# Optimization experiments

Measured on AMD Instinct MI355X. Metric: run time of the kernel, lower is better.

Reference implementation:

```python
import jax, jax.numpy as jnp
import numpy as np

B, SQ, SKV, D, H = 2, 2048, 2048, 1024, 16
DH = D // H


def setup_inputs() -> dict:
    key = jax.random.key(0)
    ks = jax.random.split(key, 4)
    s = 0.02
    return {
        "query_input": jax.random.normal(ks[0], (B, SQ, D), jnp.float32),
        "kv_input": jax.random.normal(ks[1], (B, SKV, D), jnp.float32),
        "Wq": jax.random.normal(ks[2], (D, D), jnp.float32) * s,
        "bq": jnp.zeros((D,), jnp.float32),
        "Wkv": jax.random.normal(ks[3], (D, 2 * D), jnp.float32) * s,
        "bkv": jnp.zeros((2 * D,), jnp.float32),
        "Wo": jax.random.normal(jax.random.fold_in(key, 7), (D, D), jnp.float32) * s,
        "bo": jnp.zeros((D,), jnp.float32),
    }


def reference(query_input, kv_input, Wq, bq, Wkv, bkv, Wo, bo):
    scale = 1.0 / jnp.sqrt(jnp.float32(DH))
    # Projections
    q = query_input @ Wq + bq                      # [B, SQ, D]
    kv = kv_input @ Wkv + bkv                      # [B, SKV, 2D]
    k, v = jnp.split(kv, 2, axis=-1)               # [B, SKV, D] each
    # Split heads: [B, H, S, DH]
    q = q.reshape(B, SQ, H, DH).transpose(0, 2, 1, 3)
    k = k.reshape(B, SKV, H, DH).transpose(0, 2, 1, 3)
    v = v.reshape(B, SKV, H, DH).transpose(0, 2, 1, 3)
    # Scores S = QK^T / sqrt(d_k)
    scores = jnp.einsum("bhqd,bhkd->bhqk", q, k) * scale
    attn = jax.nn.softmax(scores, axis=-1)
    out = jnp.einsum("bhqk,bhkd->bhqd", attn, v)   # [B, H, SQ, DH]
    out = out.transpose(0, 2, 1, 3).reshape(B, SQ, D)
    return out @ Wo + bo
```

## Files before the change

### kernel.cpp

```cpp
#include <hip/hip_runtime.h>

typedef unsigned short u16;
typedef unsigned int u32;
typedef __bf16 bf16x8 __attribute__((ext_vector_type(8)));
typedef __bf16 bf16x2 __attribute__((ext_vector_type(2)));
typedef float f32x4 __attribute__((ext_vector_type(4)));
typedef float f32x16 __attribute__((ext_vector_type(16)));

#define QSCALE 0.18033688011112f

__device__ __forceinline__ u16 f2bf(float f) {
  u32 u = __builtin_bit_cast(u32, f);
  u += 0x7fffu + ((u >> 16) & 1u);
  return (u16)(u >> 16);
}

__device__ __forceinline__ u32 pkbf(float a, float b) {
  bf16x2 t = {(__bf16)a, (__bf16)b};
  return __builtin_bit_cast(u32, t);
}

__device__ __forceinline__ bf16x8 as_bf16x8(uint4 v) {
  return __builtin_bit_cast(bf16x8, v);
}

__device__ __forceinline__ void async16(const void* g, void* l) {
  __builtin_amdgcn_global_load_lds(
      (__attribute__((address_space(1))) void*)(g),
      (__attribute__((address_space(3))) void*)(l), 16, 0, 0);
}

__global__ void prep_kernel(const float* __restrict__ xq, const float* __restrict__ xkv,
                            const float* __restrict__ Wq, const float* __restrict__ Wkv,
                            const float* __restrict__ Wo,
                            u16* __restrict__ Xq16, u16* __restrict__ Xkv16,
                            u16* __restrict__ WqT, u16* __restrict__ WkvT,
                            u16* __restrict__ WoT) {
  const int bid = blockIdx.x, tid = threadIdx.x;
  if (bid < 8192) {
    int i = bid * 256 + tid;
    const float* s; u16* d; int j;
    if (i < 1048576) { s = xq; d = Xq16; j = i; }
    else             { s = xkv; d = Xkv16; j = i - 1048576; }
    float4 v = ((const float4*)s)[j];
    ushort4 o;
    o.x = f2bf(v.x); o.y = f2bf(v.y); o.z = f2bf(v.z); o.w = f2bf(v.w);
    ((ushort4*)d)[j] = o;
    return;
  }
  const int b2 = bid - 8192;
  const int z = b2 >> 11, rem = b2 & 2047;
  const int by = rem >> 6, bx = rem & 63;
  const float* src; u16* dst; int Nd;
  if (z == 0)      { src = Wq;  dst = WqT;  Nd = 1024; }
  else if (z == 1) { src = Wkv; dst = WkvT; Nd = 2048; }
  else             { src = Wo;  dst = WoT;  Nd = 1024; }
  const int n0 = bx * 32, k0 = by * 32;
  if (n0 >= Nd) return;
  __shared__ float tile[32][33];
  const int tx = tid & 31, ty = tid >> 5;
#pragma unroll
  for (int j = 0; j < 4; ++j)
    tile[ty + 8 * j][tx] = src[(size_t)(k0 + ty + 8 * j) * Nd + n0 + tx];
  __syncthreads();
#pragma unroll
  for (int j = 0; j < 4; ++j)
    dst[(size_t)(n0 + ty + 8 * j) * 1024 + k0 + tx] = f2bf(tile[tx][ty + 8 * j]);
}

template <int MI>
static __device__ __forceinline__ void gemm_core(
    const u16* __restrict__ A, const u16* __restrict__ Bt, int m0,
    uint4* sA, uint4* sB, f32x4 (*acc)[4]) {
  const int tid = threadIdx.x;
  const int wv = tid >> 6, lane = tid & 63;
  const int quad = lane >> 4, l16 = lane & 15;
  const int wm = (wv >> 1) * (MI * 16), wn = (wv & 1) * 64;

  const int ib0 = wv * 128 + lane, ib1 = ib0 + 64;
  const int br0 = ib0 >> 2, bc0 = (ib0 & 3) ^ ((br0 >> 1) & 3);
  const int br1 = ib1 >> 2, bc1 = (ib1 & 3) ^ ((br1 >> 1) & 3);
  const u16* gB0 = Bt + (size_t)br0 * 1024 + bc0 * 8;
  const u16* gB1 = Bt + (size_t)br1 * 1024 + bc1 * 8;

  const int ia0 = wv * (MI * 32) + lane;
  const int ar0 = ia0 >> 2, ac0 = (ia0 & 3) ^ ((ar0 >> 1) & 3);
  const u16* gA0 = A + (size_t)(m0 + ar0) * 1024 + ac0 * 8;
  const int ia1 = ia0 + 64;
  const int ar1 = ia1 >> 2, ac1 = (ia1 & 3) ^ ((ar1 >> 1) & 3);
  const u16* gA1 = A + (size_t)(m0 + ar1) * 1024 + ac1 * 8;
  uint4* sAw = sA + wv * (MI * 32);
  uint4* sBw = sB + wv * 128;

  for (int k0 = 0; k0 < 1024; k0 += 32) {
    __syncthreads();
    async16(gA0 + k0, sAw);
    if (MI == 4) async16(gA1 + k0, sAw + 64);
    async16(gB0 + k0, sBw);
    async16(gB1 + k0, sBw + 64);
    __syncthreads();

    bf16x8 af[MI], bfr[4];
#pragma unroll
    for (int mi = 0; mi < MI; ++mi) {
      int r = wm + mi * 16 + l16;
      af[mi] = as_bf16x8(sA[r * 4 + (quad ^ ((r >> 1) & 3))]);
    }
#pragma unroll
    for (int ni = 0; ni < 4; ++ni) {
      int r = wn + ni * 16 + l16;
      bfr[ni] = as_bf16x8(sB[r * 4 + (quad ^ ((r >> 1) & 3))]);
    }
#pragma unroll
    for (int mi = 0; mi < MI; ++mi)
#pragma unroll
      for (int ni = 0; ni < 4; ++ni)
        acc[mi][ni] = __builtin_amdgcn_mfma_f32_16x16x32_bf16(
            af[mi], bfr[ni], acc[mi][ni], 0, 0, 0);
  }
}

__global__ __launch_bounds__(256, 3) void gemm_qkv(
    const u16* __restrict__ Xq, const u16* __restrict__ Xkv,
    const u16* __restrict__ WqT, const u16* __restrict__ WkvT,
    const float* __restrict__ bq, const float* __restrict__ bkv,
    u16* __restrict__ Qd, u16* __restrict__ Kd, u16* __restrict__ Vd) {
  __shared__ uint4 sA[512], sB[512];
  f32x4 acc[4][4] = {};
  const int n0 = blockIdx.x * 128, m0 = blockIdx.y * 128;
  const u16* A = (n0 < 1024) ? Xq : Xkv;
  const u16* Bt = (n0 < 1024) ? (WqT + (size_t)n0 * 1024)
                              : (WkvT + (size_t)(n0 - 1024) * 1024);
  const float* bias = (n0 < 1024) ? (bq + n0) : (bkv + (n0 - 1024));
  gemm_core<4>(A, Bt, m0, sA, sB, acc);

  const int tid = threadIdx.x, wv = tid >> 6, lane = tid & 63;
  const int quad = lane >> 4, l16 = lane & 15;
  const int wm = (wv >> 1) * 64, wn = (wv & 1) * 64;
  const int bb = m0 >> 11;
  const int gmb = m0 + wm + quad * 4;
  const int ssb = (m0 & 2047) + wm + quad * 4;
#pragma unroll
  for (int ni = 0; ni < 4; ++ni) {
    const int gn = n0 + wn + ni * 16 + l16;
    const float bvn = bias[wn + ni * 16 + l16];
    if (gn < 1024) {
      u16* base = Qd + gn;
#pragma unroll
      for (int mi = 0; mi < 4; ++mi)
#pragma unroll
        for (int r = 0; r < 4; ++r)
          base[(size_t)(gmb + mi * 16 + r) * 1024] = f2bf((acc[mi][ni][r] + bvn) * QSCALE);
    } else if (gn < 2048) {
      u16* base = Kd + (gn - 1024);
#pragma unroll
      for (int mi = 0; mi < 4; ++mi)
#pragma unroll
        for (int r = 0; r < 4; ++r)
          base[(size_t)(gmb + mi * 16 + r) * 1024] = f2bf(acc[mi][ni][r] + bvn);
    } else {
      const int col = gn - 2048, hh = col >> 6, dh = col & 63;
      u16* base = Vd + ((size_t)(bb * 16 + hh) * 64 + dh) * 2048 + ssb;
#pragma unroll
      for (int mi = 0; mi < 4; ++mi) {
        ushort4 o;
        o.x = f2bf(acc[mi][ni][0] + bvn);
        o.y = f2bf(acc[mi][ni][1] + bvn);
        o.z = f2bf(acc[mi][ni][2] + bvn);
        o.w = f2bf(acc[mi][ni][3] + bvn);
        *(ushort4*)(base + mi * 16) = o;
      }
    }
  }
}

__global__ __launch_bounds__(512, 4) void flash_attn(
    const u16* __restrict__ Q, const u16* __restrict__ K,
    const u16* __restrict__ V, u16* __restrict__ O) {
  __shared__ uint4 sbuf[4096];
  __shared__ float sLB[128];
  __shared__ float sLA[128];

  const int tid = threadIdx.x;
  const int wv = tid >> 6, lane = tid & 63;
  const int grp = wv >> 2, wq = wv & 3;
  const int c = lane & 31, hh = lane >> 5;
  const int hb = blockIdx.x & 31;
  const int q0 = (blockIdx.x >> 5) * 128;
  const int h = hb & 15, bz = hb >> 4;

  const u16* Qb = Q + ((size_t)(bz * 2048 + q0 + wq * 32)) * 1024 + h * 64;
  const u16* Kb = K + ((size_t)(bz * 2048 + grp * 64)) * 1024 + h * 64;
  const u16* Vb = V + ((size_t)(bz * 16 + h)) * 64 * 2048 + grp * 64;

  uint4* sKg = sbuf + grp * 1024;
  uint4* sVg = sbuf + 2048 + grp * 1024;

  const int i0 = wq * 128 + lane, i1 = i0 + 64;
  const int r0 = i0 >> 3, r1 = i1 >> 3;
  const int ck0 = (i0 & 7) ^ (r0 & 7), ck1 = (i1 & 7) ^ (r1 & 7);
  const u16* gK0 = Kb + (size_t)r0 * 1024 + ck0 * 8;
  const u16* gK1 = Kb + (size_t)r1 * 1024 + ck1 * 8;
  const u16* gV0 = Vb + (size_t)r0 * 2048 + ck0 * 8;
  const u16* gV1 = Vb + (size_t)r1 * 2048 + ck1 * 8;
  const int wo = wq * 128;

  bf16x8 qf[4];
  {
    const u16* qr = Qb + (size_t)c * 1024 + hh * 8;
#pragma unroll
    for (int s = 0; s < 4; ++s)
      qf[s] = as_bf16x8(*(const uint4*)(qr + 16 * s));
  }

  f32x16 oacc[2] = {};
  float lp = 0.f;

  async16(gK0, sKg + wo);
  async16(gK1, sKg + wo + 64);
  async16(gV0, sVg + wo);
  async16(gV1, sVg + wo + 64);

  for (int t = 0; t < 16; ++t) {
    const int cur = t & 1;
    __syncthreads();
    if (t < 15) {
      const size_t ko = (size_t)(t + 1) * 128 * 1024;
      const int vo = (t + 1) * 128;
      async16(gK0 + ko, sKg + (cur ^ 1) * 512 + wo);
      async16(gK1 + ko, sKg + (cur ^ 1) * 512 + wo + 64);
      async16(gV0 + vo, sVg + (cur ^ 1) * 512 + wo);
      async16(gV1 + vo, sVg + (cur ^ 1) * 512 + wo + 64);
    }
    const uint4* K_ = sKg + cur * 512;
    const uint4* V_ = sVg + cur * 512;

    bf16x8 kf[2][4];
#pragma unroll
    for (int b = 0; b < 2; ++b) {
      const int row = 32 * b + c, sw = row & 7;
#pragma unroll
      for (int s = 0; s < 4; ++s)
        kf[b][s] = as_bf16x8(K_[row * 8 + ((2 * s + hh) ^ sw)]);
    }

    bf16x8 pa[4];
#pragma unroll
    for (int b = 0; b < 2; ++b) {
      f32x16 sAcc = {};
      __builtin_amdgcn_s_setprio(1);
#pragma unroll
      for (int s = 0; s < 4; ++s)
        sAcc = __builtin_amdgcn_mfma_f32_32x32x16_bf16(kf[b][s], qf[s], sAcc, 0, 0, 0);
      __builtin_amdgcn_s_setprio(0);
      float e[16];
#pragma unroll
      for (int r = 0; r < 16; ++r) e[r] = __builtin_amdgcn_exp2f(sAcc[r]);
      float t0 = (e[0] + e[1]) + (e[2] + e[3]);
      float t1 = (e[4] + e[5]) + (e[6] + e[7]);
      float t2 = (e[8] + e[9]) + (e[10] + e[11]);
      float t3 = (e[12] + e[13]) + (e[14] + e[15]);
      lp += (t0 + t1) + (t2 + t3);
      u32 wA0 = pkbf(e[0], e[1]),   wA1 = pkbf(e[2], e[3]);
      u32 wB0 = pkbf(e[4], e[5]),   wB1 = pkbf(e[6], e[7]);
      u32 wC0 = pkbf(e[8], e[9]),   wC1 = pkbf(e[10], e[11]);
      u32 wD0 = pkbf(e[12], e[13]), wD1 = pkbf(e[14], e[15]);
      asm("v_permlane32_swap_b32 %0, %1" : "+v"(wA0), "+v"(wB0));
      asm("v_permlane32_swap_b32 %0, %1" : "+v"(wA1), "+v"(wB1));
      asm("v_permlane32_swap_b32 %0, %1" : "+v"(wC0), "+v"(wD0));
      asm("v_permlane32_swap_b32 %0, %1" : "+v"(wC1), "+v"(wD1));
      uint4 f0 = {wA0, wA1, wB0, wB1};
      uint4 f1 = {wC0, wC1, wD0, wD1};
      pa[2 * b]     = as_bf16x8(f0);
      pa[2 * b + 1] = as_bf16x8(f1);
    }

    bf16x8 vf[2][4];
#pragma unroll
    for (int nb = 0; nb < 2; ++nb) {
      const int row = 32 * nb + c, sw = row & 7;
#pragma unroll
      for (int ks = 0; ks < 4; ++ks)
        vf[nb][ks] = as_bf16x8(V_[row * 8 + ((2 * ks + hh) ^ sw)]);
    }

    __builtin_amdgcn_s_setprio(1);
#pragma unroll
    for (int nb = 0; nb < 2; ++nb)
#pragma unroll
      for (int ks = 0; ks < 4; ++ks)
        oacc[nb] = __builtin_amdgcn_mfma_f32_32x32x16_bf16(
            pa[ks], vf[nb][ks], oacc[nb], 0, 0, 0);
    __builtin_amdgcn_s_setprio(0);
  }

  float rtot;
  {
    u32 a = __builtin_bit_cast(u32, lp);
    u32 b = a;
    asm("v_permlane32_swap_b32 %0, %1" : "+v"(a), "+v"(b));
    rtot = __builtin_bit_cast(float, a) + __builtin_bit_cast(float, b);
  }
  if (grp) sLB[wq * 32 + c] = rtot;

  __syncthreads();
  float* scr = (float*)sbuf;

  if (grp) {
#pragma unroll
    for (int nb = 0; nb < 2; ++nb) {
      float* dst = scr + (wq * 2 + nb) * 1024;
#pragma unroll
      for (int r = 0; r < 16; ++r)
        dst[r * 64 + lane] = oacc[nb][r];
    }
  }
  __syncthreads();
  if (!grp) {
#pragma unroll
    for (int nb = 0; nb < 2; ++nb) {
      const float* sp = scr + (wq * 2 + nb) * 1024;
#pragma unroll
      for (int r = 0; r < 16; ++r)
        oacc[nb][r] += sp[r * 64 + lane];
    }
    float tot = rtot + sLB[wq * 32 + c];
    sLA[wq * 32 + c] = 1.0f / tot;

    u16* Ob = O + ((size_t)(bz * 2048 + q0 + wq * 32)) * 1024 + h * 64;
#pragma unroll
    for (int nb = 0; nb < 2; ++nb)
#pragma unroll
      for (int r = 0; r < 16; ++r) {
        const int qr = (r & 3) + 8 * (r >> 2) + 4 * hh;
        float rl = sLA[wq * 32 + qr];
        Ob[(size_t)qr * 1024 + nb * 32 + c] = f2bf(oacc[nb][r] * rl);
      }
  }
}

__global__ __launch_bounds__(256, 2) void gemm_out(
    const u16* __restrict__ A, const u16* __restrict__ Bt,
    const float* __restrict__ bias, float* __restrict__ C) {
  __shared__ uint4 sA[256], sB[512];
  f32x4 acc[2][4] = {};
  const int n0 = blockIdx.x * 128, m0 = blockIdx.y * 64;
  gemm_core<2>(A, Bt + (size_t)n0 * 1024, m0, sA, sB, acc);

  const int tid = threadIdx.x, wv = tid >> 6, lane = tid & 63;
  const int quad = lane >> 4, l16 = lane & 15;
  const int wm = (wv >> 1) * 32, wn = (wv & 1) * 64;
  float bv[4];
#pragma unroll
  for (int ni = 0; ni < 4; ++ni) bv[ni] = bias[n0 + wn + ni * 16 + l16];
#pragma unroll
  for (int mi = 0; mi < 2; ++mi)
#pragma unroll
    for (int ni = 0; ni < 4; ++ni)
#pragma unroll
      for (int r = 0; r < 4; ++r) {
        int gm = m0 + wm + mi * 16 + quad * 4 + r;
        int gn = n0 + wn + ni * 16 + l16;
        C[(size_t)gm * 1024 + gn] = acc[mi][ni][r] + bv[ni];
      }
}

extern "C" void kernel_launch(void* const* d_in, const int* in_sizes, int n_in,
                              void* d_out, int out_size, void* d_ws, size_t ws_size,
                              hipStream_t stream) {
  const float* xq  = (const float*)d_in[0];
  const float* xkv = (const float*)d_in[1];
  const float* Wq  = (const float*)d_in[2];
  const float* bq  = (const float*)d_in[3];
  const float* Wkv = (const float*)d_in[4];
  const float* bkv = (const float*)d_in[5];
  const float* Wo  = (const float*)d_in[6];
  const float* bo  = (const float*)d_in[7];
  float* out = (float*)d_out;

  char* p = (char*)d_ws;
  u16* Xq16  = (u16*)p; p += (size_t)8 << 20;
  u16* Xkv16 = (u16*)p; p += (size_t)8 << 20;
  u16* WqT   = (u16*)p; p += (size_t)2 << 20;
  u16* WkvT  = (u16*)p; p += (size_t)4 << 20;
  u16* WoT   = (u16*)p; p += (size_t)2 << 20;
  u16* Q16   = (u16*)p; p += (size_t)8 << 20;
  u16* K16   = (u16*)p; p += (size_t)8 << 20;
  u16* Vt16  = (u16*)p; p += (size_t)8 << 20;
  u16* O16   = (u16*)p; p += (size_t)8 << 20;

  prep_kernel<<<14336, 256, 0, stream>>>(xq, xkv, Wq, Wkv, Wo,
                                         Xq16, Xkv16, WqT, WkvT, WoT);
  gemm_qkv<<<dim3(24, 32), 256, 0, stream>>>(Xq16, Xkv16, WqT, WkvT, bq, bkv,
                                             Q16, K16, Vt16);
  flash_attn<<<512, 512, 0, stream>>>(Q16, K16, Vt16, O16);
  gemm_out<<<dim3(8, 64), 256, 0, stream>>>(O16, WoT, bo, out);
}
```

Baseline: 196.4 us.

## Load K/V directly from global into registers, drop LDS staging and split-KV groups

The flash attention kernel no longer stages K and V tiles through shared memory with async copies and a two-group split over the KV range. Each of four waves now streams its own K/V fragments from global memory straight into registers, prefetching the next 64-key tile one iteration ahead. This removes the per-tile barriers and the final cross-group reduction through LDS. In exchange, each wave issues redundant global loads of K/V that the four waves used to share, relying on L2/L1 hits, and the block shrinks to 256 threads with higher register pressure from the double-buffered fragments.

```diff
diff --git a/kernel.cpp b/kernel.cpp
--- a/kernel.cpp
+++ b/kernel.cpp
@@ -174,40 +174,25 @@
   }
 }
 
-__global__ __launch_bounds__(512, 4) void flash_attn(
+__global__ __launch_bounds__(256, 2) void flash_attn(
     const u16* __restrict__ Q, const u16* __restrict__ K,
     const u16* __restrict__ V, u16* __restrict__ O) {
-  __shared__ uint4 sbuf[4096];
-  __shared__ float sLB[128];
-  __shared__ float sLA[128];
+  __shared__ float sL[128];
 
   const int tid = threadIdx.x;
-  const int wv = tid >> 6, lane = tid & 63;
-  const int grp = wv >> 2, wq = wv & 3;
+  const int wq = tid >> 6, lane = tid & 63;
   const int c = lane & 31, hh = lane >> 5;
   const int hb = blockIdx.x & 31;
   const int q0 = (blockIdx.x >> 5) * 128;
   const int h = hb & 15, bz = hb >> 4;
 
   const u16* Qb = Q + ((size_t)(bz * 2048 + q0 + wq * 32)) * 1024 + h * 64;
-  const u16* Kb = K + ((size_t)(bz * 2048 + grp * 64)) * 1024 + h * 64;
-  const u16* Vb = V + ((size_t)(bz * 16 + h)) * 64 * 2048 + grp * 64;
-
-  uint4* sKg = sbuf + grp * 1024;
-  uint4* sVg = sbuf + 2048 + grp * 1024;
-
-  const int i0 = wq * 128 + lane, i1 = i0 + 64;
-  const int r0 = i0 >> 3, r1 = i1 >> 3;
-  const int ck0 = (i0 & 7) ^ (r0 & 7), ck1 = (i1 & 7) ^ (r1 & 7);
-  const u16* gK0 = Kb + (size_t)r0 * 1024 + ck0 * 8;
-  const u16* gK1 = Kb + (size_t)r1 * 1024 + ck1 * 8;
-  const u16* gV0 = Vb + (size_t)r0 * 2048 + ck0 * 8;
-  const u16* gV1 = Vb + (size_t)r1 * 2048 + ck1 * 8;
-  const int wo = wq * 128;
+  const u16* kRow = K + ((size_t)(bz * 2048 + c)) * 1024 + h * 64 + 8 * hh;
+  const u16* vRow = V + ((size_t)(bz * 16 + h)) * 64 * 2048 + (size_t)c * 2048 + 8 * hh;
 
   bf16x8 qf[4];
   {
-    const u16* qr = Qb + (size_t)c * 1024 + hh * 8;
+    const u16* qr = Qb + (size_t)c * 1024 + 8 * hh;
 #pragma unroll
     for (int s = 0; s < 4; ++s)
       qf[s] = as_bf16x8(*(const uint4*)(qr + 16 * s));
@@ -216,32 +201,28 @@
   f32x16 oacc[2] = {};
   float lp = 0.f;
 
-  async16(gK0, sKg + wo);
-  async16(gK1, sKg + wo + 64);
-  async16(gV0, sVg + wo);
-  async16(gV1, sVg + wo + 64);
-
-  for (int t = 0; t < 16; ++t) {
-    const int cur = t & 1;
-    __syncthreads();
-    if (t < 15) {
-      const size_t ko = (size_t)(t + 1) * 128 * 1024;
-      const int vo = (t + 1) * 128;
-      async16(gK0 + ko, sKg + (cur ^ 1) * 512 + wo);
-      async16(gK1 + ko, sKg + (cur ^ 1) * 512 + wo + 64);
-      async16(gV0 + vo, sVg + (cur ^ 1) * 512 + wo);
-      async16(gV1 + vo, sVg + (cur ^ 1) * 512 + wo + 64);
-    }
-    const uint4* K_ = sKg + cur * 512;
-    const uint4* V_ = sVg + cur * 512;
-
-    bf16x8 kf[2][4];
-#pragma unroll
-    for (int b = 0; b < 2; ++b) {
-      const int row = 32 * b + c, sw = row & 7;
-#pragma unroll
-      for (int s = 0; s < 4; ++s)
-        kf[b][s] = as_bf16x8(K_[row * 8 + ((2 * s + hh) ^ sw)]);
+  bf16x8 kf[2][4], vf[2][4];
+#pragma unroll
+  for (int b = 0; b < 2; ++b)
+#pragma unroll
+    for (int s = 0; s < 4; ++s) {
+      kf[b][s] = as_bf16x8(*(const uint4*)(kRow + (size_t)(32 * b) * 1024 + 16 * s));
+      vf[b][s] = as_bf16x8(*(const uint4*)(vRow + (size_t)(32 * b) * 2048 + 16 * s));
+    }
+
+#pragma unroll 2
+  for (int t = 0; t < 32; ++t) {
+    bf16x8 kn[2][4], vn[2][4];
+    if (t < 31) {
+      const u16* kN = kRow + (size_t)(64 * (t + 1)) * 1024;
+      const u16* vN = vRow + 64 * (t + 1);
+#pragma unroll
+      for (int b = 0; b < 2; ++b)
+#pragma unroll
+        for (int s = 0; s < 4; ++s) {
+          kn[b][s] = as_bf16x8(*(const uint4*)(kN + (size_t)(32 * b) * 1024 + 16 * s));
+          vn[b][s] = as_bf16x8(*(const uint4*)(vN + (size_t)(32 * b) * 2048 + 16 * s));
+        }
     }
 
     bf16x8 pa[4];
@@ -275,15 +256,6 @@
       pa[2 * b + 1] = as_bf16x8(f1);
     }
 
-    bf16x8 vf[2][4];
-#pragma unroll
-    for (int nb = 0; nb < 2; ++nb) {
-      const int row = 32 * nb + c, sw = row & 7;
-#pragma unroll
-      for (int ks = 0; ks < 4; ++ks)
-        vf[nb][ks] = as_bf16x8(V_[row * 8 + ((2 * ks + hh) ^ sw)]);
-    }
-
     __builtin_amdgcn_s_setprio(1);
 #pragma unroll
     for (int nb = 0; nb < 2; ++nb)
@@ -292,51 +264,30 @@
         oacc[nb] = __builtin_amdgcn_mfma_f32_32x32x16_bf16(
             pa[ks], vf[nb][ks], oacc[nb], 0, 0, 0);
     __builtin_amdgcn_s_setprio(0);
-  }
-
-  float rtot;
+
+#pragma unroll
+    for (int b = 0; b < 2; ++b)
+#pragma unroll
+      for (int s = 0; s < 4; ++s) { kf[b][s] = kn[b][s]; vf[b][s] = vn[b][s]; }
+  }
+
   {
     u32 a = __builtin_bit_cast(u32, lp);
     u32 b = a;
     asm("v_permlane32_swap_b32 %0, %1" : "+v"(a), "+v"(b));
-    rtot = __builtin_bit_cast(float, a) + __builtin_bit_cast(float, b);
-  }
-  if (grp) sLB[wq * 32 + c] = rtot;
-
-  __syncthreads();
-  float* scr = (float*)sbuf;
-
-  if (grp) {
-#pragma unroll
-    for (int nb = 0; nb < 2; ++nb) {
-      float* dst = scr + (wq * 2 + nb) * 1024;
-#pragma unroll
-      for (int r = 0; r < 16; ++r)
-        dst[r * 64 + lane] = oacc[nb][r];
-    }
-  }
-  __syncthreads();
-  if (!grp) {
-#pragma unroll
-    for (int nb = 0; nb < 2; ++nb) {
-      const float* sp = scr + (wq * 2 + nb) * 1024;
-#pragma unroll
-      for (int r = 0; r < 16; ++r)
-        oacc[nb][r] += sp[r * 64 + lane];
-    }
-    float tot = rtot + sLB[wq * 32 + c];
-    sLA[wq * 32 + c] = 1.0f / tot;
-
-    u16* Ob = O + ((size_t)(bz * 2048 + q0 + wq * 32)) * 1024 + h * 64;
-#pragma unroll
-    for (int nb = 0; nb < 2; ++nb)
-#pragma unroll
-      for (int r = 0; r < 16; ++r) {
-        const int qr = (r & 3) + 8 * (r >> 2) + 4 * hh;
-        float rl = sLA[wq * 32 + qr];
-        Ob[(size_t)qr * 1024 + nb * 32 + c] = f2bf(oacc[nb][r] * rl);
-      }
-  }
+    float tot = __builtin_bit_cast(float, a) + __builtin_bit_cast(float, b);
+    sL[wq * 32 + c] = 1.0f / tot;
+  }
+
+  u16* Ob = O + ((size_t)(bz * 2048 + q0 + wq * 32)) * 1024 + h * 64;
+#pragma unroll
+  for (int nb = 0; nb < 2; ++nb)
+#pragma unroll
+    for (int r = 0; r < 16; ++r) {
+      const int qr = (r & 3) + 8 * (r >> 2) + 4 * hh;
+      float rl = sL[wq * 32 + qr];
+      Ob[(size_t)qr * 1024 + nb * 32 + c] = f2bf(oacc[nb][r] * rl);
+    }
 }
 
 __global__ __launch_bounds__(256, 2) void gemm_out(
@@ -393,6 +344,6 @@
                                          Xq16, Xkv16, WqT, WkvT, WoT);
   gemm_qkv<<<dim3(24, 32), 256, 0, stream>>>(Xq16, Xkv16, WqT, WkvT, bq, bkv,
                                              Q16, K16, Vt16);
-  flash_attn<<<512, 512, 0, stream>>>(Q16, K16, Vt16, O16);
+  flash_attn<<<512, 256, 0, stream>>>(Q16, K16, Vt16, O16);
   gemm_out<<<dim3(8, 64), 256, 0, stream>>>(O16, WoT, bo, out);
 }
```

Result: slower. 270.1 us (+37.5%).
